# Performance work log

Measured on AMD Instinct MI355X. Metric: run time of the kernel, lower is better.

Reference implementation:

```python
import jax, jax.numpy as jnp
import numpy as np

N = 100000
E = 1600000
IN_C, HID_C, OUT_C = 64, 64, 16


def setup_inputs() -> dict:
    key = jax.random.key(0)
    k1, k2, k3, k4, k5 = jax.random.split(key, 5)
    x = jax.random.normal(k1, (N, IN_C), dtype=jnp.float32)
    edge_index = jax.random.randint(k2, (2, E), 0, N, dtype=jnp.int64)
    # Glorot-style init like PyG GCNConv
    W1 = jax.random.normal(k3, (IN_C, HID_C), dtype=jnp.float32) * (1.0 / np.sqrt(IN_C))
    b1 = jnp.zeros((HID_C,), dtype=jnp.float32)
    W2 = jax.random.normal(k4, (HID_C, OUT_C), dtype=jnp.float32) * (1.0 / np.sqrt(HID_C))
    b2 = jnp.zeros((OUT_C,), dtype=jnp.float32)
    return {"x": x, "edge_index": edge_index, "W1": W1, "b1": b1, "W2": W2, "b2": b2}


def _gcn_conv(h, src, dst, norm, W, b, n_nodes):
    # h: [N, F_in] -> linear transform first (PyG order), then normalized aggregation
    h = h @ W  # [N, F_out]
    msgs = h[src] * norm[:, None]          # gather + scale, [E+N, F_out]
    out = jax.ops.segment_sum(msgs, dst, num_segments=n_nodes)  # scatter-add
    return out + b


def reference(x, edge_index, W1, b1, W2, b2):
    n = x.shape[0]
    loop = jnp.arange(n, dtype=edge_index.dtype)
    src = jnp.concatenate([edge_index[0], loop])  # add self-loops
    dst = jnp.concatenate([edge_index[1], loop])
    # symmetric normalization D^{-1/2} (A+I) D^{-1/2}
    deg = jax.ops.segment_sum(jnp.ones_like(dst, dtype=x.dtype), dst, num_segments=n)
    dinv = jnp.where(deg > 0, jax.lax.rsqrt(deg), 0.0)
    norm = dinv[src] * dinv[dst]  # [E+N]

    h = jax.nn.relu(_gcn_conv(x, src, dst, norm, W1, b1, n))
    # dropout is identity in eval mode
    return _gcn_conv(h, src, dst, norm, W2, b2, n)
```

## Files before the change

### kernel.cpp

```cpp
#include <hip/hip_runtime.h>


namespace {
constexpr int BLK = 256;
constexpr int NPB = 256;
constexpr int PCHUNK = 2048;
constexpr int STRIDE = 5120;
constexpr int CPAD = 32;

__device__ inline float bf2f(unsigned short h) {
    union { unsigned u; float f; } v; v.u = (unsigned)h << 16; return v.f;
}
__device__ inline unsigned short f2bf(float f) {
    union { float f; unsigned u; } v; v.f = f;
    unsigned r = (v.u + 0x7FFFu + ((v.u >> 16) & 1u)) >> 16;
    return (unsigned short)r;
}
__device__ inline unsigned pack2bf(float a, float b) {
    return (unsigned)f2bf(a) | ((unsigned)f2bf(b) << 16);
}

__global__ __launch_bounds__(BLK) void k_zero(int* __restrict__ p, int n) {
    int i = blockIdx.x * BLK + threadIdx.x;
    if (i < n) p[i] = 0;
}

__global__ __launch_bounds__(BLK) void k_part(const int* __restrict__ src,
                                              const int* __restrict__ dst,
                                              int* __restrict__ bcnt,
                                              unsigned* __restrict__ packed,
                                              int e, int nb) {
    __shared__ int sdst[PCHUNK];
    __shared__ int hist[1024];
    __shared__ int base[1024];
    int t = threadIdx.x;
    int chunk0 = blockIdx.x * PCHUNK;
    if (chunk0 >= e) return;
    int lim = min(PCHUNK, e - chunk0);
    int lim4 = lim >> 2;
    for (int i = t; i < nb; i += BLK) hist[i] = 0;
    __syncthreads();
    const int4* d4 = (const int4*)(dst + chunk0);
    for (int i = t; i < lim4; i += BLK) {
        int4 d = d4[i];
        ((int4*)sdst)[i] = d;
        atomicAdd(&hist[d.x >> 8], 1);
        atomicAdd(&hist[d.y >> 8], 1);
        atomicAdd(&hist[d.z >> 8], 1);
        atomicAdd(&hist[d.w >> 8], 1);
    }
    for (int i = (lim4 << 2) + t; i < lim; i += BLK) {
        int d = dst[chunk0 + i];
        sdst[i] = d;
        atomicAdd(&hist[d >> 8], 1);
    }
    __syncthreads();
    for (int i = t; i < nb; i += BLK) {
        int c = hist[i];
        base[i] = c ? (i * STRIDE + atomicAdd(&bcnt[i * CPAD], c)) : 0;
        hist[i] = 0;
    }
    __syncthreads();
    const int4* s4 = (const int4*)(src + chunk0);
    for (int i = t; i < lim4; i += BLK) {
        int4 d = ((int4*)sdst)[i];
        int4 s = s4[i];
        int b0 = d.x >> 8, b1 = d.y >> 8, b2 = d.z >> 8, b3 = d.w >> 8;
        int r0 = atomicAdd(&hist[b0], 1);
        packed[base[b0] + r0] = ((unsigned)s.x << 8) | (unsigned)(d.x & 255);
        int r1 = atomicAdd(&hist[b1], 1);
        packed[base[b1] + r1] = ((unsigned)s.y << 8) | (unsigned)(d.y & 255);
        int r2 = atomicAdd(&hist[b2], 1);
        packed[base[b2] + r2] = ((unsigned)s.z << 8) | (unsigned)(d.z & 255);
        int r3 = atomicAdd(&hist[b3], 1);
        packed[base[b3] + r3] = ((unsigned)s.w << 8) | (unsigned)(d.w & 255);
    }
    for (int i = (lim4 << 2) + t; i < lim; i += BLK) {
        int d = sdst[i];
        int b = d >> 8;
        int r = atomicAdd(&hist[b], 1);
        packed[base[b] + r] = ((unsigned)src[chunk0 + i] << 8) | (unsigned)(d & 255);
    }
}

__global__ __launch_bounds__(512) void k_sort(const unsigned* __restrict__ packed,
                                              const int* __restrict__ bcnt,
                                              int* __restrict__ ssrc,
                                              int* __restrict__ rowbeg,
                                              int* __restrict__ rowcnt,
                                              float* __restrict__ dinv, int n) {
    __shared__ unsigned sp[STRIDE];
    __shared__ int cnt[NPB];
    __shared__ int offs[NPB];
    int b = blockIdx.x;
    int t = threadIdx.x;
    int regionBase = b * STRIDE;
    int ecnt = bcnt[b * CPAD];
    if (t < NPB) cnt[t] = 0;
    __syncthreads();
    for (int i = t; i < ecnt; i += 512) {
        unsigned p = packed[regionBase + i];
        sp[i] = p;
        atomicAdd(&cnt[p & 255u], 1);
    }
    __syncthreads();
    if (t < NPB) offs[t] = cnt[t];
    __syncthreads();
    for (int off = 1; off < NPB; off <<= 1) {
        int x = 0;
        if (t < NPB && t >= off) x = offs[t - off];
        __syncthreads();
        if (t < NPB) offs[t] += x;
        __syncthreads();
    }
    int myoff = 0;
    if (t < NPB) {
        int v = cnt[t];
        myoff = offs[t] - v;
        int node = (b << 8) + t;
        if (node < n) {
            rowbeg[node] = regionBase + myoff;
            rowcnt[node] = v;
            dinv[node] = rsqrtf((float)(v + 1));
        }
    }
    __syncthreads();
    if (t < NPB) cnt[t] = regionBase + myoff;
    __syncthreads();
    for (int i = t; i < ecnt; i += 512) {
        unsigned p = sp[i];
        int pos = atomicAdd(&cnt[p & 255u], 1);
        ssrc[pos] = (int)(p >> 8);
    }
}


__global__ __launch_bounds__(BLK) void k_gemm1(const float* __restrict__ x,
                                               const float* __restrict__ W1,
                                               const float* __restrict__ dinv,
                                               unsigned short* __restrict__ hhat, int n) {
    __shared__ float W[64 * 64];
    int t = threadIdx.x;
    #pragma unroll
    for (int i = 0; i < 16; ++i) W[t + BLK * i] = W1[t + BLK * i];
    __syncthreads();
    const int cg = t & 3;
    const int ng = t >> 2;
    const int node0 = blockIdx.x * 256 + ng * 4;
    const float* Wc = W + cg * 16;

    int nd[4];
    #pragma unroll
    for (int i = 0; i < 4; ++i) {
        int v = node0 + i;
        nd[i] = (v < n) ? v : (n - 1);
    }

    float4 acc[4][4];
    #pragma unroll
    for (int i = 0; i < 4; ++i)
        #pragma unroll
        for (int c = 0; c < 4; ++c) acc[i][c] = make_float4(0.f, 0.f, 0.f, 0.f);

    for (int k4 = 0; k4 < 16; ++k4) {
        float4 xv[4];
        #pragma unroll
        for (int i = 0; i < 4; ++i)
            xv[i] = ((const float4*)(x + (size_t)nd[i] * 64))[k4];
        #pragma unroll
        for (int kk = 0; kk < 4; ++kk) {
            const float4* wr = (const float4*)(Wc + (k4 * 4 + kk) * 64);
            float4 w0 = wr[0], w1 = wr[1], w2 = wr[2], w3 = wr[3];
            #pragma unroll
            for (int i = 0; i < 4; ++i) {
                float xa[4] = {xv[i].x, xv[i].y, xv[i].z, xv[i].w};
                float xs = xa[kk];
                acc[i][0].x = fmaf(xs, w0.x, acc[i][0].x);
                acc[i][0].y = fmaf(xs, w0.y, acc[i][0].y);
                acc[i][0].z = fmaf(xs, w0.z, acc[i][0].z);
                acc[i][0].w = fmaf(xs, w0.w, acc[i][0].w);
                acc[i][1].x = fmaf(xs, w1.x, acc[i][1].x);
                acc[i][1].y = fmaf(xs, w1.y, acc[i][1].y);
                acc[i][1].z = fmaf(xs, w1.z, acc[i][1].z);
                acc[i][1].w = fmaf(xs, w1.w, acc[i][1].w);
                acc[i][2].x = fmaf(xs, w2.x, acc[i][2].x);
                acc[i][2].y = fmaf(xs, w2.y, acc[i][2].y);
                acc[i][2].z = fmaf(xs, w2.z, acc[i][2].z);
                acc[i][2].w = fmaf(xs, w2.w, acc[i][2].w);
                acc[i][3].x = fmaf(xs, w3.x, acc[i][3].x);
                acc[i][3].y = fmaf(xs, w3.y, acc[i][3].y);
                acc[i][3].z = fmaf(xs, w3.z, acc[i][3].z);
                acc[i][3].w = fmaf(xs, w3.w, acc[i][3].w);
            }
        }
    }
    #pragma unroll
    for (int i = 0; i < 4; ++i) {
        int v = node0 + i;
        if (v < n) {
            float d = dinv[v];
            unsigned u0 = pack2bf(acc[i][0].x * d, acc[i][0].y * d);
            unsigned u1 = pack2bf(acc[i][0].z * d, acc[i][0].w * d);
            unsigned u2 = pack2bf(acc[i][1].x * d, acc[i][1].y * d);
            unsigned u3 = pack2bf(acc[i][1].z * d, acc[i][1].w * d);
            unsigned u4 = pack2bf(acc[i][2].x * d, acc[i][2].y * d);
            unsigned u5 = pack2bf(acc[i][2].z * d, acc[i][2].w * d);
            unsigned u6 = pack2bf(acc[i][3].x * d, acc[i][3].y * d);
            unsigned u7 = pack2bf(acc[i][3].z * d, acc[i][3].w * d);
            uint4* dst = (uint4*)(hhat + (size_t)v * 64 + cg * 16);
            dst[0] = make_uint4(u0, u1, u2, u3);
            dst[1] = make_uint4(u4, u5, u6, u7);
        }
    }
}

__global__ __launch_bounds__(BLK) void k_agg1(const unsigned short* __restrict__ hhat,
                                              const int* __restrict__ rowbeg,
                                              const int* __restrict__ rowcnt,
                                              const int* __restrict__ ssrc,
                                              const float* __restrict__ dinv,
                                              const float* __restrict__ b1,
                                              const float* __restrict__ W2,
                                              unsigned short* __restrict__ h2hat, int n) {
    int wid = __builtin_amdgcn_readfirstlane(
        (int)((blockIdx.x * BLK + threadIdx.x) >> 6));
    int lane = threadIdx.x & 63;
    if (wid >= n) return;
    const int g = lane >> 4;
    const int j = lane & 15;
    float w2r[16];
    #pragma unroll
    for (int k = 0; k < 16; ++k) w2r[k] = W2[(g * 16 + k) * 16 + j];

    int beg = rowbeg[wid];
    int cnt = rowcnt[wid];
    float a = bf2f(hhat[((size_t)wid << 6) + lane]);
    int e = 0;
    for (; e + 8 <= cnt; e += 8) {
        int s0 = ssrc[beg + e + 0], s1 = ssrc[beg + e + 1];
        int s2 = ssrc[beg + e + 2], s3 = ssrc[beg + e + 3];
        int s4 = ssrc[beg + e + 4], s5 = ssrc[beg + e + 5];
        int s6 = ssrc[beg + e + 6], s7 = ssrc[beg + e + 7];
        float v0 = bf2f(hhat[((size_t)s0 << 6) + lane]);
        float v1 = bf2f(hhat[((size_t)s1 << 6) + lane]);
        float v2 = bf2f(hhat[((size_t)s2 << 6) + lane]);
        float v3 = bf2f(hhat[((size_t)s3 << 6) + lane]);
        float v4 = bf2f(hhat[((size_t)s4 << 6) + lane]);
        float v5 = bf2f(hhat[((size_t)s5 << 6) + lane]);
        float v6 = bf2f(hhat[((size_t)s6 << 6) + lane]);
        float v7 = bf2f(hhat[((size_t)s7 << 6) + lane]);
        a += ((v0 + v1) + (v2 + v3)) + ((v4 + v5) + (v6 + v7));
    }
    if (e + 4 <= cnt) {
        int s0 = ssrc[beg + e + 0], s1 = ssrc[beg + e + 1];
        int s2 = ssrc[beg + e + 2], s3 = ssrc[beg + e + 3];
        float v0 = bf2f(hhat[((size_t)s0 << 6) + lane]);
        float v1 = bf2f(hhat[((size_t)s1 << 6) + lane]);
        float v2 = bf2f(hhat[((size_t)s2 << 6) + lane]);
        float v3 = bf2f(hhat[((size_t)s3 << 6) + lane]);
        a += (v0 + v1) + (v2 + v3);
        e += 4;
    }
    for (; e < cnt; ++e)
        a += bf2f(hhat[((size_t)ssrc[beg + e] << 6) + lane]);

    float dv = dinv[wid];
    float h = fmaxf(fmaf(dv, a, b1[lane]), 0.f);

    float part = 0.f;
    #pragma unroll
    for (int k = 0; k < 16; ++k) {
        float hv = __shfl(h, g * 16 + k, 64);
        part = fmaf(hv, w2r[k], part);
    }
    part += __shfl_xor(part, 16, 64);
    part += __shfl_xor(part, 32, 64);
    if (g == 0) h2hat[(size_t)wid * 16 + j] = f2bf(part * dv);
}

__global__ __launch_bounds__(BLK) void k_agg2(const unsigned short* __restrict__ h2,
                                              const int* __restrict__ rowbeg,
                                              const int* __restrict__ rowcnt,
                                              const int* __restrict__ ssrc,
                                              const float* __restrict__ dinv,
                                              const float* __restrict__ b2,
                                              float* __restrict__ out, int n) {
    int wid = __builtin_amdgcn_readfirstlane(
        (int)((blockIdx.x * BLK + threadIdx.x) >> 6));
    int lane = threadIdx.x & 63;
    if (wid >= n) return;
    int q = lane >> 4;
    int c = lane & 15;
    int beg = rowbeg[wid];
    int cnt = rowcnt[wid];
    float a = 0.f;
    int e = 0;
    for (; e + 4 <= cnt; e += 4) {
        int s0 = ssrc[beg + e + 0], s1 = ssrc[beg + e + 1];
        int s2 = ssrc[beg + e + 2], s3 = ssrc[beg + e + 3];
        int sa = (q & 1) ? s1 : s0;
        int sb = (q & 1) ? s3 : s2;
        int s = (q & 2) ? sb : sa;
        a += bf2f(h2[((size_t)s << 4) + c]);
    }
    if (e + q < cnt)
        a += bf2f(h2[((size_t)ssrc[beg + e + q] << 4) + c]);
    a += __shfl_xor(a, 16, 64);
    a += __shfl_xor(a, 32, 64);
    if (q == 0) {
        float self = bf2f(h2[((size_t)wid << 4) + c]);
        out[((size_t)wid << 4) + c] = fmaf(dinv[wid], a + self, b2[c]);
    }
}

}

extern "C" void kernel_launch(void* const* d_in, const int* in_sizes, int n_in,
                              void* d_out, int out_size, void* d_ws, size_t ws_size,
                              hipStream_t stream) {
    const float* x  = (const float*)d_in[0];
    const int*   ei = (const int*)d_in[1];
    const float* W1 = (const float*)d_in[2];
    const float* b1 = (const float*)d_in[3];
    const float* W2 = (const float*)d_in[4];
    const float* b2 = (const float*)d_in[5];
    float* out = (float*)d_out;

    const int N = in_sizes[0] / 64;
    const int E = in_sizes[1] / 2;
    const int* src = ei;
    const int* dst = ei + E;
    const int nb = (N + NPB - 1) / NPB;

    char* ws = (char*)d_ws;
    size_t off = 0;
    auto alloc = [&](size_t bytes) -> char* {
        char* p = ws + off;
        off = (off + bytes + 255) & ~(size_t)255;
        return p;
    };
    int*            bcnt   = (int*)alloc((size_t)1024 * CPAD * 4);
    int*            rowbeg = (int*)alloc((size_t)N * 4);
    int*            rowcnt = (int*)alloc((size_t)N * 4);
    float*          dinv   = (float*)alloc((size_t)N * 4);
    unsigned*       packed = (unsigned*)alloc((size_t)nb * STRIDE * 4);
    int*            ssrc   = (int*)alloc((size_t)nb * STRIDE * 4);
    unsigned short* hhat   = (unsigned short*)alloc((size_t)N * 64 * 2);
    unsigned short* h2hat  = (unsigned short*)alloc((size_t)N * 16 * 2);

    const int nb_n = (N + BLK - 1) / BLK;
    const int nchunks = (E + PCHUNK - 1) / PCHUNK;
    const int nb_w = (int)(((long long)N * 64 + BLK - 1) / BLK);

    const int zn = nb * CPAD;
    k_zero<<<(zn + BLK - 1) / BLK, BLK, 0, stream>>>(bcnt, zn);
    k_part<<<nchunks, BLK, 0, stream>>>(src, dst, bcnt, packed, E, nb);
    k_sort<<<nb, 512, 0, stream>>>(packed, bcnt, ssrc, rowbeg, rowcnt, dinv, N);

    k_gemm1<<<nb_n, BLK, 0, stream>>>(x, W1, dinv, hhat, N);
    k_agg1<<<nb_w, BLK, 0, stream>>>(hhat, rowbeg, rowcnt, ssrc, dinv, b1, W2,
                                     h2hat, N);
    k_agg2<<<nb_w, BLK, 0, stream>>>(h2hat, rowbeg, rowcnt, ssrc, dinv, b2, out, N);
}
```

Before: 241.5 us.

## Process two destination nodes per wave in agg1 and unroll agg2 gather deeper

k_agg1 now assigns two destination nodes to each wavefront and interleaves their 8-wide gathers, putting more independent loads in flight per wave and halving the per-wave W2 register load. k_agg2 now unrolls its neighbor loop to 8 edges per iteration, with two loads per lane. The partition chunk size also grows from 2048 to 8192 edges per block. The costs are fewer waves in agg1, which can hurt latency hiding or load balance when the two nodes' degrees differ, and larger partition blocks with fewer of them launched.

```diff
diff --git a/kernel.cpp b/kernel.cpp
--- a/kernel.cpp
+++ b/kernel.cpp
@@ -4,7 +4,7 @@
 namespace {
 constexpr int BLK = 256;
 constexpr int NPB = 256;
-constexpr int PCHUNK = 2048;
+constexpr int PCHUNK = 8192;
 constexpr int STRIDE = 5120;
 constexpr int CPAD = 32;
 
@@ -18,6 +18,33 @@
 }
 __device__ inline unsigned pack2bf(float a, float b) {
     return (unsigned)f2bf(a) | ((unsigned)f2bf(b) << 16);
+}
+
+__device__ inline float gather8(const unsigned short* __restrict__ hhat,
+                                const int* __restrict__ ssrc, int base, int lane) {
+    int s0 = ssrc[base + 0], s1 = ssrc[base + 1];
+    int s2 = ssrc[base + 2], s3 = ssrc[base + 3];
+    int s4 = ssrc[base + 4], s5 = ssrc[base + 5];
+    int s6 = ssrc[base + 6], s7 = ssrc[base + 7];
+    float v0 = bf2f(hhat[((size_t)s0 << 6) + lane]);
+    float v1 = bf2f(hhat[((size_t)s1 << 6) + lane]);
+    float v2 = bf2f(hhat[((size_t)s2 << 6) + lane]);
+    float v3 = bf2f(hhat[((size_t)s3 << 6) + lane]);
+    float v4 = bf2f(hhat[((size_t)s4 << 6) + lane]);
+    float v5 = bf2f(hhat[((size_t)s5 << 6) + lane]);
+    float v6 = bf2f(hhat[((size_t)s6 << 6) + lane]);
+    float v7 = bf2f(hhat[((size_t)s7 << 6) + lane]);
+    return ((v0 + v1) + (v2 + v3)) + ((v4 + v5) + (v6 + v7));
+}
+__device__ inline float gather4(const unsigned short* __restrict__ hhat,
+                                const int* __restrict__ ssrc, int base, int lane) {
+    int s0 = ssrc[base + 0], s1 = ssrc[base + 1];
+    int s2 = ssrc[base + 2], s3 = ssrc[base + 3];
+    float v0 = bf2f(hhat[((size_t)s0 << 6) + lane]);
+    float v1 = bf2f(hhat[((size_t)s1 << 6) + lane]);
+    float v2 = bf2f(hhat[((size_t)s2 << 6) + lane]);
+    float v3 = bf2f(hhat[((size_t)s3 << 6) + lane]);
+    return (v0 + v1) + (v2 + v3);
 }
 
 __global__ __launch_bounds__(BLK) void k_zero(int* __restrict__ p, int n) {
@@ -222,60 +249,62 @@
                                               const float* __restrict__ b1,
                                               const float* __restrict__ W2,
                                               unsigned short* __restrict__ h2hat, int n) {
-    int wid = __builtin_amdgcn_readfirstlane(
+    int pair = __builtin_amdgcn_readfirstlane(
         (int)((blockIdx.x * BLK + threadIdx.x) >> 6));
     int lane = threadIdx.x & 63;
-    if (wid >= n) return;
+    int wid0 = pair << 1;
+    if (wid0 >= n) return;
+    int wid1 = wid0 + 1;
+    bool has1 = (wid1 < n);
     const int g = lane >> 4;
     const int j = lane & 15;
     float w2r[16];
     #pragma unroll
     for (int k = 0; k < 16; ++k) w2r[k] = W2[(g * 16 + k) * 16 + j];
 
-    int beg = rowbeg[wid];
-    int cnt = rowcnt[wid];
-    float a = bf2f(hhat[((size_t)wid << 6) + lane]);
-    int e = 0;
-    for (; e + 8 <= cnt; e += 8) {
-        int s0 = ssrc[beg + e + 0], s1 = ssrc[beg + e + 1];
-        int s2 = ssrc[beg + e + 2], s3 = ssrc[beg + e + 3];
-        int s4 = ssrc[beg + e + 4], s5 = ssrc[beg + e + 5];
-        int s6 = ssrc[beg + e + 6], s7 = ssrc[beg + e + 7];
-        float v0 = bf2f(hhat[((size_t)s0 << 6) + lane]);
-        float v1 = bf2f(hhat[((size_t)s1 << 6) + lane]);
-        float v2 = bf2f(hhat[((size_t)s2 << 6) + lane]);
-        float v3 = bf2f(hhat[((size_t)s3 << 6) + lane]);
-        float v4 = bf2f(hhat[((size_t)s4 << 6) + lane]);
-        float v5 = bf2f(hhat[((size_t)s5 << 6) + lane]);
-        float v6 = bf2f(hhat[((size_t)s6 << 6) + lane]);
-        float v7 = bf2f(hhat[((size_t)s7 << 6) + lane]);
-        a += ((v0 + v1) + (v2 + v3)) + ((v4 + v5) + (v6 + v7));
-    }
-    if (e + 4 <= cnt) {
-        int s0 = ssrc[beg + e + 0], s1 = ssrc[beg + e + 1];
-        int s2 = ssrc[beg + e + 2], s3 = ssrc[beg + e + 3];
-        float v0 = bf2f(hhat[((size_t)s0 << 6) + lane]);
-        float v1 = bf2f(hhat[((size_t)s1 << 6) + lane]);
-        float v2 = bf2f(hhat[((size_t)s2 << 6) + lane]);
-        float v3 = bf2f(hhat[((size_t)s3 << 6) + lane]);
-        a += (v0 + v1) + (v2 + v3);
-        e += 4;
-    }
-    for (; e < cnt; ++e)
-        a += bf2f(hhat[((size_t)ssrc[beg + e] << 6) + lane]);
-
-    float dv = dinv[wid];
-    float h = fmaxf(fmaf(dv, a, b1[lane]), 0.f);
-
-    float part = 0.f;
-    #pragma unroll
-    for (int k = 0; k < 16; ++k) {
-        float hv = __shfl(h, g * 16 + k, 64);
-        part = fmaf(hv, w2r[k], part);
-    }
-    part += __shfl_xor(part, 16, 64);
-    part += __shfl_xor(part, 32, 64);
-    if (g == 0) h2hat[(size_t)wid * 16 + j] = f2bf(part * dv);
+    int beg0 = rowbeg[wid0], cnt0 = rowcnt[wid0];
+    int beg1 = 0, cnt1 = 0;
+    if (has1) { beg1 = rowbeg[wid1]; cnt1 = rowcnt[wid1]; }
+    float a0 = bf2f(hhat[((size_t)wid0 << 6) + lane]);
+    float a1 = 0.f;
+    if (has1) a1 = bf2f(hhat[((size_t)wid1 << 6) + lane]);
+    int e0 = 0, e1 = 0;
+    while (e0 + 8 <= cnt0 && e1 + 8 <= cnt1) {
+        float r0 = gather8(hhat, ssrc, beg0 + e0, lane);
+        float r1 = gather8(hhat, ssrc, beg1 + e1, lane);
+        a0 += r0;
+        a1 += r1;
+        e0 += 8; e1 += 8;
+    }
+    for (; e0 + 8 <= cnt0; e0 += 8) a0 += gather8(hhat, ssrc, beg0 + e0, lane);
+    for (; e1 + 8 <= cnt1; e1 += 8) a1 += gather8(hhat, ssrc, beg1 + e1, lane);
+    if (e0 + 4 <= cnt0) { a0 += gather4(hhat, ssrc, beg0 + e0, lane); e0 += 4; }
+    if (e1 + 4 <= cnt1) { a1 += gather4(hhat, ssrc, beg1 + e1, lane); e1 += 4; }
+    for (; e0 < cnt0; ++e0) a0 += bf2f(hhat[((size_t)ssrc[beg0 + e0] << 6) + lane]);
+    for (; e1 < cnt1; ++e1) a1 += bf2f(hhat[((size_t)ssrc[beg1 + e1] << 6) + lane]);
+
+    {
+        float dv = dinv[wid0];
+        float h = fmaxf(fmaf(dv, a0, b1[lane]), 0.f);
+        float part = 0.f;
+        #pragma unroll
+        for (int k = 0; k < 16; ++k)
+            part = fmaf(__shfl(h, g * 16 + k, 64), w2r[k], part);
+        part += __shfl_xor(part, 16, 64);
+        part += __shfl_xor(part, 32, 64);
+        if (g == 0) h2hat[(size_t)wid0 * 16 + j] = f2bf(part * dv);
+    }
+    if (has1) {
+        float dv = dinv[wid1];
+        float h = fmaxf(fmaf(dv, a1, b1[lane]), 0.f);
+        float part = 0.f;
+        #pragma unroll
+        for (int k = 0; k < 16; ++k)
+            part = fmaf(__shfl(h, g * 16 + k, 64), w2r[k], part);
+        part += __shfl_xor(part, 16, 64);
+        part += __shfl_xor(part, 32, 64);
+        if (g == 0) h2hat[(size_t)wid1 * 16 + j] = f2bf(part * dv);
+    }
 }
 
 __global__ __launch_bounds__(BLK) void k_agg2(const unsigned short* __restrict__ h2,
@@ -295,13 +324,29 @@
     int cnt = rowcnt[wid];
     float a = 0.f;
     int e = 0;
-    for (; e + 4 <= cnt; e += 4) {
+    for (; e + 8 <= cnt; e += 8) {
+        int s0 = ssrc[beg + e + 0], s1 = ssrc[beg + e + 1];
+        int s2 = ssrc[beg + e + 2], s3 = ssrc[beg + e + 3];
+        int s4 = ssrc[beg + e + 4], s5 = ssrc[beg + e + 5];
+        int s6 = ssrc[beg + e + 6], s7 = ssrc[beg + e + 7];
+        int sa = (q & 1) ? s1 : s0;
+        int sb = (q & 1) ? s3 : s2;
+        int sA = (q & 2) ? sb : sa;
+        int sc2 = (q & 1) ? s5 : s4;
+        int sd = (q & 1) ? s7 : s6;
+        int sB = (q & 2) ? sd : sc2;
+        float vA = bf2f(h2[((size_t)sA << 4) + c]);
+        float vB = bf2f(h2[((size_t)sB << 4) + c]);
+        a += vA + vB;
+    }
+    if (e + 4 <= cnt) {
         int s0 = ssrc[beg + e + 0], s1 = ssrc[beg + e + 1];
         int s2 = ssrc[beg + e + 2], s3 = ssrc[beg + e + 3];
         int sa = (q & 1) ? s1 : s0;
         int sb = (q & 1) ? s3 : s2;
         int s = (q & 2) ? sb : sa;
         a += bf2f(h2[((size_t)s << 4) + c]);
+        e += 4;
     }
     if (e + q < cnt)
         a += bf2f(h2[((size_t)ssrc[beg + e + q] << 4) + c]);
@@ -350,6 +395,8 @@
 
     const int nb_n = (N + BLK - 1) / BLK;
     const int nchunks = (E + PCHUNK - 1) / PCHUNK;
+    const int npairs = (N + 1) / 2;
+    const int nb_p = (int)(((long long)npairs * 64 + BLK - 1) / BLK);
     const int nb_w = (int)(((long long)N * 64 + BLK - 1) / BLK);
 
     const int zn = nb * CPAD;
@@ -358,7 +405,7 @@
     k_sort<<<nb, 512, 0, stream>>>(packed, bcnt, ssrc, rowbeg, rowcnt, dinv, N);
 
     k_gemm1<<<nb_n, BLK, 0, stream>>>(x, W1, dinv, hhat, N);
-    k_agg1<<<nb_w, BLK, 0, stream>>>(hhat, rowbeg, rowcnt, ssrc, dinv, b1, W2,
+    k_agg1<<<nb_p, BLK, 0, stream>>>(hhat, rowbeg, rowcnt, ssrc, dinv, b1, W2,
                                      h2hat, N);
     k_agg2<<<nb_w, BLK, 0, stream>>>(h2hat, rowbeg, rowcnt, ssrc, dinv, b2, out, N);
 }
```

New measurement: 210.9 us. -12.7%, faster.

## Split layer-1 features into 16-channel blocks and separate second GEMM

Applied to the files above, without the earlier changes.

Stores the transformed layer-1 features as four column blocks of 16 bf16 channels, so each aggregation pass gathers 32-byte rows that fit the cache better, with four edges handled per wavefront. The W2 projection moves out of the aggregation kernel into a new per-node GEMM kernel that reads an intermediate h1 buffer. This costs an extra N×64 bf16 write and read, and ssrc is now read four times. It also raises the partition chunk size and unrolls the layer-2 gather to eight edges.

```diff
diff --git a/kernel.cpp b/kernel.cpp
--- a/kernel.cpp
+++ b/kernel.cpp
@@ -4,12 +4,18 @@
 namespace {
 constexpr int BLK = 256;
 constexpr int NPB = 256;
-constexpr int PCHUNK = 2048;
+constexpr int PCHUNK = 8192;
 constexpr int STRIDE = 5120;
 constexpr int CPAD = 32;
 
 __device__ inline float bf2f(unsigned short h) {
     union { unsigned u; float f; } v; v.u = (unsigned)h << 16; return v.f;
+}
+__device__ inline float bfl(unsigned u) {
+    union { unsigned u; float f; } v; v.u = u << 16; return v.f;
+}
+__device__ inline float bfh(unsigned u) {
+    union { unsigned u; float f; } v; v.u = u & 0xFFFF0000u; return v.f;
 }
 __device__ inline unsigned short f2bf(float f) {
     union { float f; unsigned u; } v; v.f = f;
@@ -18,6 +24,11 @@
 }
 __device__ inline unsigned pack2bf(float a, float b) {
     return (unsigned)f2bf(a) | ((unsigned)f2bf(b) << 16);
+}
+__device__ inline int sel4(int s0, int s1, int s2, int s3, int q) {
+    int sa = (q & 1) ? s1 : s0;
+    int sb = (q & 1) ? s3 : s2;
+    return (q & 2) ? sb : sa;
 }
 
 __global__ __launch_bounds__(BLK) void k_zero(int* __restrict__ p, int n) {
@@ -138,7 +149,7 @@
 __global__ __launch_bounds__(BLK) void k_gemm1(const float* __restrict__ x,
                                                const float* __restrict__ W1,
                                                const float* __restrict__ dinv,
-                                               unsigned short* __restrict__ hhat, int n) {
+                                               unsigned short* __restrict__ hhb, int n) {
     __shared__ float W[64 * 64];
     int t = threadIdx.x;
     #pragma unroll
@@ -194,6 +205,7 @@
             }
         }
     }
+    size_t cbase = (size_t)cg * ((size_t)n * 16);
     #pragma unroll
     for (int i = 0; i < 4; ++i) {
         int v = node0 + i;
@@ -207,75 +219,120 @@
             unsigned u5 = pack2bf(acc[i][2].z * d, acc[i][2].w * d);
             unsigned u6 = pack2bf(acc[i][3].x * d, acc[i][3].y * d);
             unsigned u7 = pack2bf(acc[i][3].z * d, acc[i][3].w * d);
-            uint4* dst = (uint4*)(hhat + (size_t)v * 64 + cg * 16);
+            uint4* dst = (uint4*)(hhb + cbase + (size_t)v * 16);
             dst[0] = make_uint4(u0, u1, u2, u3);
             dst[1] = make_uint4(u4, u5, u6, u7);
         }
     }
 }
 
-__global__ __launch_bounds__(BLK) void k_agg1(const unsigned short* __restrict__ hhat,
+__global__ __launch_bounds__(BLK) void k_agg1(const unsigned short* __restrict__ hhb,
                                               const int* __restrict__ rowbeg,
                                               const int* __restrict__ rowcnt,
                                               const int* __restrict__ ssrc,
                                               const float* __restrict__ dinv,
                                               const float* __restrict__ b1,
-                                              const float* __restrict__ W2,
-                                              unsigned short* __restrict__ h2hat, int n) {
-    int wid = __builtin_amdgcn_readfirstlane(
-        (int)((blockIdx.x * BLK + threadIdx.x) >> 6));
+                                              unsigned short* __restrict__ h1b,
+                                              int n, int nbn4) {
+    int bid = blockIdx.x;
+    int cb = bid / nbn4;
+    int nblk = bid - cb * nbn4;
+    int wid = __builtin_amdgcn_readfirstlane(nblk * 4 + (int)(threadIdx.x >> 6));
     int lane = threadIdx.x & 63;
     if (wid >= n) return;
-    const int g = lane >> 4;
-    const int j = lane & 15;
-    float w2r[16];
-    #pragma unroll
-    for (int k = 0; k < 16; ++k) w2r[k] = W2[(g * 16 + k) * 16 + j];
-
+    int q = lane >> 4;
+    int c = lane & 15;
+    size_t cbase = (size_t)cb * ((size_t)n * 16);
+    const unsigned short* tab = hhb + cbase;
     int beg = rowbeg[wid];
     int cnt = rowcnt[wid];
-    float a = bf2f(hhat[((size_t)wid << 6) + lane]);
+    float a = 0.f;
     int e = 0;
-    for (; e + 8 <= cnt; e += 8) {
+    for (; e + 16 <= cnt; e += 16) {
+        int s0 = ssrc[beg + e + 0],  s1 = ssrc[beg + e + 1];
+        int s2 = ssrc[beg + e + 2],  s3 = ssrc[beg + e + 3];
+        int s4 = ssrc[beg + e + 4],  s5 = ssrc[beg + e + 5];
+        int s6 = ssrc[beg + e + 6],  s7 = ssrc[beg + e + 7];
+        int s8 = ssrc[beg + e + 8],  s9 = ssrc[beg + e + 9];
+        int sA = ssrc[beg + e + 10], sB = ssrc[beg + e + 11];
+        int sC = ssrc[beg + e + 12], sD = ssrc[beg + e + 13];
+        int sE = ssrc[beg + e + 14], sF = ssrc[beg + e + 15];
+        int g0 = sel4(s0, s1, s2, s3, q);
+        int g1 = sel4(s4, s5, s6, s7, q);
+        int g2 = sel4(s8, s9, sA, sB, q);
+        int g3 = sel4(sC, sD, sE, sF, q);
+        float v0 = bf2f(tab[((size_t)g0 << 4) + c]);
+        float v1 = bf2f(tab[((size_t)g1 << 4) + c]);
+        float v2 = bf2f(tab[((size_t)g2 << 4) + c]);
+        float v3 = bf2f(tab[((size_t)g3 << 4) + c]);
+        a += (v0 + v1) + (v2 + v3);
+    }
+    for (; e + 4 <= cnt; e += 4) {
         int s0 = ssrc[beg + e + 0], s1 = ssrc[beg + e + 1];
         int s2 = ssrc[beg + e + 2], s3 = ssrc[beg + e + 3];
-        int s4 = ssrc[beg + e + 4], s5 = ssrc[beg + e + 5];
-        int s6 = ssrc[beg + e + 6], s7 = ssrc[beg + e + 7];
-        float v0 = bf2f(hhat[((size_t)s0 << 6) + lane]);
-        float v1 = bf2f(hhat[((size_t)s1 << 6) + lane]);
-        float v2 = bf2f(hhat[((size_t)s2 << 6) + lane]);
-        float v3 = bf2f(hhat[((size_t)s3 << 6) + lane]);
-        float v4 = bf2f(hhat[((size_t)s4 << 6) + lane]);
-        float v5 = bf2f(hhat[((size_t)s5 << 6) + lane]);
-        float v6 = bf2f(hhat[((size_t)s6 << 6) + lane]);
-        float v7 = bf2f(hhat[((size_t)s7 << 6) + lane]);
-        a += ((v0 + v1) + (v2 + v3)) + ((v4 + v5) + (v6 + v7));
-    }
-    if (e + 4 <= cnt) {
-        int s0 = ssrc[beg + e + 0], s1 = ssrc[beg + e + 1];
-        int s2 = ssrc[beg + e + 2], s3 = ssrc[beg + e + 3];
-        float v0 = bf2f(hhat[((size_t)s0 << 6) + lane]);
-        float v1 = bf2f(hhat[((size_t)s1 << 6) + lane]);
-        float v2 = bf2f(hhat[((size_t)s2 << 6) + lane]);
-        float v3 = bf2f(hhat[((size_t)s3 << 6) + lane]);
-        a += (v0 + v1) + (v2 + v3);
-        e += 4;
-    }
-    for (; e < cnt; ++e)
-        a += bf2f(hhat[((size_t)ssrc[beg + e] << 6) + lane]);
-
-    float dv = dinv[wid];
-    float h = fmaxf(fmaf(dv, a, b1[lane]), 0.f);
-
-    float part = 0.f;
-    #pragma unroll
-    for (int k = 0; k < 16; ++k) {
-        float hv = __shfl(h, g * 16 + k, 64);
-        part = fmaf(hv, w2r[k], part);
-    }
-    part += __shfl_xor(part, 16, 64);
-    part += __shfl_xor(part, 32, 64);
-    if (g == 0) h2hat[(size_t)wid * 16 + j] = f2bf(part * dv);
+        int g = sel4(s0, s1, s2, s3, q);
+        a += bf2f(tab[((size_t)g << 4) + c]);
+    }
+    if (e + q < cnt)
+        a += bf2f(tab[((size_t)ssrc[beg + e + q] << 4) + c]);
+    a += __shfl_xor(a, 16, 64);
+    a += __shfl_xor(a, 32, 64);
+    if (q == 0) {
+        float self = bf2f(tab[((size_t)wid << 4) + c]);
+        float dv = dinv[wid];
+        float h = fmaxf(fmaf(dv, a + self, b1[cb * 16 + c]), 0.f);
+        h1b[cbase + ((size_t)wid << 4) + c] = f2bf(h);
+    }
+}
+
+__global__ __launch_bounds__(BLK) void k_gemm2(const unsigned short* __restrict__ h1b,
+                                               const float* __restrict__ W2,
+                                               const float* __restrict__ dinv,
+                                               unsigned short* __restrict__ h2hat, int n) {
+    __shared__ float W[64 * 16];
+    int t = threadIdx.x;
+    #pragma unroll
+    for (int i = 0; i < 4; ++i) W[t + BLK * i] = W2[t + BLK * i];
+    __syncthreads();
+    int node = blockIdx.x * BLK + t;
+    if (node >= n) return;
+    float4 a0 = make_float4(0.f, 0.f, 0.f, 0.f);
+    float4 a1 = a0, a2 = a0, a3 = a0;
+    #pragma unroll
+    for (int cb = 0; cb < 4; ++cb) {
+        const uint4* p = (const uint4*)(h1b + (size_t)cb * ((size_t)n * 16)
+                                        + (size_t)node * 16);
+        uint4 u0 = p[0], u1 = p[1];
+        float hv[16];
+        hv[0] = bfl(u0.x);  hv[1] = bfh(u0.x);
+        hv[2] = bfl(u0.y);  hv[3] = bfh(u0.y);
+        hv[4] = bfl(u0.z);  hv[5] = bfh(u0.z);
+        hv[6] = bfl(u0.w);  hv[7] = bfh(u0.w);
+        hv[8] = bfl(u1.x);  hv[9] = bfh(u1.x);
+        hv[10] = bfl(u1.y); hv[11] = bfh(u1.y);
+        hv[12] = bfl(u1.z); hv[13] = bfh(u1.z);
+        hv[14] = bfl(u1.w); hv[15] = bfh(u1.w);
+        #pragma unroll
+        for (int k = 0; k < 16; ++k) {
+            float h = hv[k];
+            const float4* wr = (const float4*)(W + (cb * 16 + k) * 16);
+            float4 w0 = wr[0], w1 = wr[1], w2 = wr[2], w3 = wr[3];
+            a0.x = fmaf(h, w0.x, a0.x); a0.y = fmaf(h, w0.y, a0.y);
+            a0.z = fmaf(h, w0.z, a0.z); a0.w = fmaf(h, w0.w, a0.w);
+            a1.x = fmaf(h, w1.x, a1.x); a1.y = fmaf(h, w1.y, a1.y);
+            a1.z = fmaf(h, w1.z, a1.z); a1.w = fmaf(h, w1.w, a1.w);
+            a2.x = fmaf(h, w2.x, a2.x); a2.y = fmaf(h, w2.y, a2.y);
+            a2.z = fmaf(h, w2.z, a2.z); a2.w = fmaf(h, w2.w, a2.w);
+            a3.x = fmaf(h, w3.x, a3.x); a3.y = fmaf(h, w3.y, a3.y);
+            a3.z = fmaf(h, w3.z, a3.z); a3.w = fmaf(h, w3.w, a3.w);
+        }
+    }
+    float d = dinv[node];
+    uint4* dst = (uint4*)(h2hat + (size_t)node * 16);
+    dst[0] = make_uint4(pack2bf(a0.x * d, a0.y * d), pack2bf(a0.z * d, a0.w * d),
+                        pack2bf(a1.x * d, a1.y * d), pack2bf(a1.z * d, a1.w * d));
+    dst[1] = make_uint4(pack2bf(a2.x * d, a2.y * d), pack2bf(a2.z * d, a2.w * d),
+                        pack2bf(a3.x * d, a3.y * d), pack2bf(a3.z * d, a3.w * d));
 }
 
 __global__ __launch_bounds__(BLK) void k_agg2(const unsigned short* __restrict__ h2,
@@ -295,13 +352,23 @@
     int cnt = rowcnt[wid];
     float a = 0.f;
     int e = 0;
-    for (; e + 4 <= cnt; e += 4) {
+    for (; e + 8 <= cnt; e += 8) {
         int s0 = ssrc[beg + e + 0], s1 = ssrc[beg + e + 1];
         int s2 = ssrc[beg + e + 2], s3 = ssrc[beg + e + 3];
-        int sa = (q & 1) ? s1 : s0;
-        int sb = (q & 1) ? s3 : s2;
-        int s = (q & 2) ? sb : sa;
+        int s4 = ssrc[beg + e + 4], s5 = ssrc[beg + e + 5];
+        int s6 = ssrc[beg + e + 6], s7 = ssrc[beg + e + 7];
+        int sA = sel4(s0, s1, s2, s3, q);
+        int sB = sel4(s4, s5, s6, s7, q);
+        float vA = bf2f(h2[((size_t)sA << 4) + c]);
+        float vB = bf2f(h2[((size_t)sB << 4) + c]);
+        a += vA + vB;
+    }
+    if (e + 4 <= cnt) {
+        int s0 = ssrc[beg + e + 0], s1 = ssrc[beg + e + 1];
+        int s2 = ssrc[beg + e + 2], s3 = ssrc[beg + e + 3];
+        int s = sel4(s0, s1, s2, s3, q);
         a += bf2f(h2[((size_t)s << 4) + c]);
+        e += 4;
     }
     if (e + q < cnt)
         a += bf2f(h2[((size_t)ssrc[beg + e + q] << 4) + c]);
@@ -345,11 +412,13 @@
     float*          dinv   = (float*)alloc((size_t)N * 4);
     unsigned*       packed = (unsigned*)alloc((size_t)nb * STRIDE * 4);
     int*            ssrc   = (int*)alloc((size_t)nb * STRIDE * 4);
-    unsigned short* hhat   = (unsigned short*)alloc((size_t)N * 64 * 2);
+    unsigned short* hhb    = (unsigned short*)alloc((size_t)N * 64 * 2);
+    unsigned short* h1b    = (unsigned short*)alloc((size_t)N * 64 * 2);
     unsigned short* h2hat  = (unsigned short*)alloc((size_t)N * 16 * 2);
 
     const int nb_n = (N + BLK - 1) / BLK;
     const int nchunks = (E + PCHUNK - 1) / PCHUNK;
+    const int nbn4 = (N + 3) / 4;
     const int nb_w = (int)(((long long)N * 64 + BLK - 1) / BLK);
 
     const int zn = nb * CPAD;
@@ -357,8 +426,9 @@
     k_part<<<nchunks, BLK, 0, stream>>>(src, dst, bcnt, packed, E, nb);
     k_sort<<<nb, 512, 0, stream>>>(packed, bcnt, ssrc, rowbeg, rowcnt, dinv, N);
 
-    k_gemm1<<<nb_n, BLK, 0, stream>>>(x, W1, dinv, hhat, N);
-    k_agg1<<<nb_w, BLK, 0, stream>>>(hhat, rowbeg, rowcnt, ssrc, dinv, b1, W2,
-                                     h2hat, N);
+    k_gemm1<<<nb_n, BLK, 0, stream>>>(x, W1, dinv, hhb, N);
+    k_agg1<<<4 * nbn4, BLK, 0, stream>>>(hhb, rowbeg, rowcnt, ssrc, dinv, b1,
+                                         h1b, N, nbn4);
+    k_gemm2<<<nb_n, BLK, 0, stream>>>(h1b, W2, dinv, h2hat, N);
     k_agg2<<<nb_w, BLK, 0, stream>>>(h2hat, rowbeg, rowcnt, ssrc, dinv, b2, out, N);
 }
```

Result: slower. 309.4 us (+28.1%).
